# Optimization experiments

Hardware: AMD Instinct MI355X
Metric: run time of the kernel (lower is better)

## Reference

```python
import jax, jax.numpy as jnp
import numpy as np

N_NODES = 100000
N_EDGES = 3200000
D = 256
REPEAT = 2
FACTOR = 0.5


def setup_inputs() -> dict:
    key = jax.random.key(0)
    k1, k2, k3, k4, k5, k6 = jax.random.split(key, 6)
    x = jax.random.normal(k1, (N_NODES, D), dtype=jnp.float32)
    vals = jax.random.uniform(k2, (N_EDGES,), dtype=jnp.float32)
    # Xavier-ish scale for linear weights
    W0 = jax.random.normal(k3, (D, D), dtype=jnp.float32) / np.sqrt(D)
    W1 = jax.random.normal(k4, (D, D), dtype=jnp.float32) / np.sqrt(D)
    rows = jax.random.randint(k5, (N_EDGES,), 0, N_NODES, dtype=jnp.int32)
    cols = jax.random.randint(k6, (N_EDGES,), 0, N_NODES, dtype=jnp.int32)
    return {"x": x, "vals": vals, "W0": W0, "W1": W1, "rows": rows, "cols": cols}


def reference(x, vals, W0, W1, rows, cols):
    # support is sparse [N, N] in COO: support[rows[e], cols[e]] = vals[e]
    def spmm(h):
        # gather source-node features, scale by edge weight, scatter-add to dst
        return jax.ops.segment_sum(vals[:, None] * h[cols], rows,
                                   num_segments=N_NODES)

    h = x
    for W, act in ((W0, jax.nn.relu), (W1, lambda v: v)):
        # _propagate: repeated SpMM with scalar factor
        for _ in range(REPEAT):
            h = spmm(h) * FACTOR
        # linear (no bias) + activation
        h = act(h @ W)
    return h
```

## Files before the change

kernel.cpp:

```cpp
#include <hip/hip_runtime.h>
#include <hip/hip_bf16.h>
#include <hip/hip_fp16.h>

#define N_D 256
#define NBLK 832

typedef __attribute__((ext_vector_type(8))) short bf16x8;
typedef __attribute__((ext_vector_type(4))) float f32x4;
typedef __attribute__((ext_vector_type(2))) float f32x2;
typedef __attribute__((ext_vector_type(2))) int   i32x2;

__device__ __forceinline__ unsigned short f2bf(float f) {
  union { float f; unsigned u; } c; c.f = f;
  unsigned u = c.u;
  return (unsigned short)((u + 0x7fffu + ((u >> 16) & 1u)) >> 16);
}
__device__ __forceinline__ float asf(unsigned u) {
  union { unsigned u; float f; } c; c.u = u;
  return c.f;
}
__device__ __forceinline__ int grp_of(int r, unsigned gmagic) {
  int g = (int)(((unsigned long long)(unsigned)r * gmagic) >> 37);
  return min(g, 7);
}

__global__ __launch_bounds__(256) void count_kernel(
    const int* __restrict__ rows, int* __restrict__ cnt8, int* __restrict__ cntT,
    int n_edges, unsigned gmagic, int M) {
  __shared__ int lcnt[8];
  if (threadIdx.x < 8) lcnt[threadIdx.x] = 0;
  __syncthreads();
  int* __restrict__ cnt = cnt8 + (size_t)(blockIdx.x & 7) * M;
  for (int e = blockIdx.x * 256 + threadIdx.x; e < n_edges; e += NBLK * 256) {
    const int r = __builtin_nontemporal_load(&rows[e]);
    atomicAdd(&cnt[r], 1);
    atomicAdd(&lcnt[grp_of(r, gmagic)], 1);
  }
  __syncthreads();
  if (threadIdx.x < 8) cntT[threadIdx.x * NBLK + blockIdx.x] = lcnt[threadIdx.x];
}

__global__ __launch_bounds__(256) void sumcnt_kernel(
    const int* __restrict__ cnt8, int* __restrict__ cnts,
    int* __restrict__ bsum, int M) {
  __shared__ int wred[4];
  const int i = blockIdx.x * 256 + threadIdx.x;
  int s = 0;
  if (i < M) {
#pragma unroll
    for (int k = 0; k < 8; ++k) s += cnt8[(size_t)k * M + i];
    cnts[i] = s;
  }
  int t = s;
#pragma unroll
  for (int off = 32; off; off >>= 1) t += __shfl_down(t, off, 64);
  if ((threadIdx.x & 63) == 0) wred[threadIdx.x >> 6] = t;
  __syncthreads();
  if (threadIdx.x == 0) bsum[blockIdx.x] = wred[0] + wred[1] + wred[2] + wred[3];
}

__global__ __launch_bounds__(1024) void scan_kernel(
    const int* __restrict__ cnt, int* __restrict__ outA,
    int* __restrict__ outB, int n) {
  __shared__ int wsum[16];
  __shared__ int carry_sh;
  const int tid = threadIdx.x;
  const int lane = tid & 63;
  const int wid = tid >> 6;
  if (tid == 0) carry_sh = 0;
  __syncthreads();
  for (int base = 0; base < n; base += 4096) {
    const int i0 = base + tid * 4;
    int4 v = make_int4(0, 0, 0, 0);
    if (i0 + 3 < n) v = *reinterpret_cast<const int4*>(cnt + i0);
    else {
      if (i0     < n) v.x = cnt[i0];
      if (i0 + 1 < n) v.y = cnt[i0 + 1];
      if (i0 + 2 < n) v.z = cnt[i0 + 2];
    }
    const int s1 = v.x, s2 = s1 + v.y, s3 = s2 + v.z, s4 = s3 + v.w;
    int ws = s4;
#pragma unroll
    for (int off = 1; off < 64; off <<= 1) {
      int o = __shfl_up(ws, off, 64);
      if (lane >= off) ws += o;
    }
    if (lane == 63) wsum[wid] = ws;
    __syncthreads();
    if (wid == 0) {
      int t = (lane < 16) ? wsum[lane] : 0;
#pragma unroll
      for (int off = 1; off < 16; off <<= 1) {
        int o = __shfl_up(t, off, 64);
        if (lane >= off) t += o;
      }
      if (lane < 16) wsum[lane] = t;
    }
    __syncthreads();
    const int carry = carry_sh;
    const int tbase = carry + (wid ? wsum[wid - 1] : 0) + ws - s4;
    if (i0     < n) { outA[i0]     = tbase;      outB[i0]     = tbase; }
    if (i0 + 1 < n) { outA[i0 + 1] = tbase + s1; outB[i0 + 1] = tbase + s1; }
    if (i0 + 2 < n) { outA[i0 + 2] = tbase + s2; outB[i0 + 2] = tbase + s2; }
    if (i0 + 3 < n) { outA[i0 + 3] = tbase + s3; outB[i0 + 3] = tbase + s3; }
    __syncthreads();
    if (tid == 0) carry_sh = carry + wsum[15];
    __syncthreads();
  }
  if (tid == 0) outA[n] = carry_sh;
}

__global__ __launch_bounds__(256) void scan_apply_kernel(
    const int* __restrict__ cnts, const int* __restrict__ bofs,
    int* __restrict__ row_ptr, int* __restrict__ cursor, int M) {
  __shared__ int wsum[4];
  const int tid = threadIdx.x;
  const int lane = tid & 63;
  const int wid = tid >> 6;
  const int i = blockIdx.x * 256 + tid;
  const int v = (i < M) ? cnts[i] : 0;
  int s = v;
#pragma unroll
  for (int off = 1; off < 64; off <<= 1) {
    int o = __shfl_up(s, off, 64);
    if (lane >= off) s += o;
  }
  if (lane == 63) wsum[wid] = s;
  __syncthreads();
  int add = 0;
  for (int k = 0; k < wid; ++k) add += wsum[k];
  const int excl = bofs[blockIdx.x] + add + s - v;
  if (i < M) { row_ptr[i] = excl; cursor[i] = excl; }
  if (i == M) row_ptr[M] = bofs[gridDim.x];
}

__global__ __launch_bounds__(256) void partition_kernel(
    const int* __restrict__ rows, const int* __restrict__ cols,
    const float* __restrict__ vals, const int* __restrict__ pofsT,
    i32x2* __restrict__ part, int n_edges, unsigned gmagic) {
  __shared__ int lofs[8];
  if (threadIdx.x < 8) lofs[threadIdx.x] = pofsT[threadIdx.x * NBLK + blockIdx.x];
  __syncthreads();
  for (int e = blockIdx.x * 256 + threadIdx.x; e < n_edges; e += NBLK * 256) {
    const int r = __builtin_nontemporal_load(&rows[e]);
    const int c = __builtin_nontemporal_load(&cols[e]);
    const float vl = __builtin_nontemporal_load(&vals[e]);
    const int g = grp_of(r, gmagic);
    const int slot = atomicAdd(&lofs[g], 1);
    const unsigned short hb = __half_as_ushort(__float2half_rn(vl * 0.5f));
    i32x2 rv;
    rv.x = r;
    rv.y = (int)(((unsigned)c << 15) | ((unsigned)hb >> 1));
    __builtin_nontemporal_store(rv, &part[slot]);
  }
}

__global__ __launch_bounds__(256) void scatter2_kernel(
    const i32x2* __restrict__ part, const int* __restrict__ pofsT,
    int* __restrict__ cursor, unsigned* __restrict__ colpack) {
  const int g  = blockIdx.x & 7;
  const int bk = blockIdx.x >> 3;
  const int nb = gridDim.x >> 3;
  const int s0 = pofsT[g * NBLK];
  const int s1 = pofsT[(g + 1) * NBLK];
  for (int i = s0 + bk * 256 + threadIdx.x; i < s1; i += nb * 256) {
    const i32x2 rv = __builtin_nontemporal_load(&part[i]);
    const int pos = atomicAdd(&cursor[rv.x], 1);
    colpack[pos] = (unsigned)rv.y;
  }
}

template <bool RELU, bool F32OUT>
__global__ __launch_bounds__(256) void spmm_slice(
    const unsigned short* __restrict__ hin, const int* __restrict__ row_ptr,
    const unsigned* __restrict__ colpack, void* __restrict__ hout,
    int n_nodes) {
  const int slice = blockIdx.x & 3;
  const int lane = threadIdx.x & 63;
  const int half = lane >> 5;
  const int sub  = lane & 31;
  const int wgid = ((blockIdx.x >> 2) * 256 + threadIdx.x) >> 6;
  const int node = wgid * 2 + half;
  const bool ok = node < n_nodes;
  int start = 0, end = 0;
  if (ok) { start = row_ptr[node]; end = row_ptr[node + 1]; }

  const unsigned* __restrict__ hinw = reinterpret_cast<const unsigned*>(hin);
  const int fofs = slice * 32 + sub;
  const int sbase = half << 5;

  float acc0 = 0.f, acc1 = 0.f;

  for (int base = start; base < end; base += 32) {
    const int cnt = min(32, end - base);
    unsigned u = 0;
    if (base + sub < end) u = __builtin_nontemporal_load(&colpack[base + sub]);
    for (int t = 0; t < cnt; t += 16) {
      unsigned hv[16];
      float v[16];
#pragma unroll
      for (int j = 0; j < 16; ++j) {
        const unsigned ue = (unsigned)__shfl((int)u, sbase + t + j, 64);
        const int c = (int)(ue >> 15);
        v[j] = __half2float(__ushort_as_half((unsigned short)((ue & 0x7fffu) << 1)));
        hv[j] = hinw[(size_t)c * 128 + fofs];
      }
#pragma unroll
      for (int j = 0; j < 16; ++j) {
        acc0 += v[j] * asf(hv[j] << 16);
        acc1 += v[j] * asf(hv[j] & 0xffff0000u);
      }
    }
  }
  if (ok) {
    if (RELU) { acc0 = fmaxf(acc0, 0.f); acc1 = fmaxf(acc1, 0.f); }
    if (F32OUT) {
      f32x2 o; o.x = acc0; o.y = acc1;
      __builtin_nontemporal_store(o, reinterpret_cast<f32x2*>(hout) + (size_t)node * 128 + fofs);
    } else {
      unsigned o = (unsigned)f2bf(acc0) | ((unsigned)f2bf(acc1) << 16);
      __builtin_nontemporal_store(o, reinterpret_cast<unsigned*>(hout) + (size_t)node * 128 + fofs);
    }
  }
}

__global__ __launch_bounds__(256) void wconv_kernel(
    const float* __restrict__ W0, const float* __restrict__ W1,
    unsigned short* __restrict__ WT0, unsigned short* __restrict__ WT1) {
  const int w = blockIdx.x >> 8;
  const int k = blockIdx.x & 255;
  const int n = threadIdx.x;
  const float* W = w ? W1 : W0;
  unsigned short* WT = w ? WT1 : WT0;
  WT[(size_t)n * N_D + k] = f2bf(W[(size_t)k * N_D + n]);
}

template <bool AF32>
__global__ __launch_bounds__(256) void gemm2(
    const void* __restrict__ H, const unsigned short* __restrict__ WT,
    unsigned short* __restrict__ C, int M) {
  const int wave = threadIdx.x >> 6;
  const int lane = threadIdx.x & 63;
  const int m = lane & 15;
  const int p = lane >> 4;
  const int row0 = blockIdx.x * 64 + wave * 16;

  f32x4 acc[16];
#pragma unroll
  for (int i = 0; i < 16; ++i) acc[i] = (f32x4){0.f, 0.f, 0.f, 0.f};

  const int r = row0 + m;
  const bool rok = r < M;

  for (int k0 = 0; k0 < N_D; k0 += 32) {
    bf16x8 a = {0, 0, 0, 0, 0, 0, 0, 0};
    if (rok) {
      if (AF32) {
        const float* ap = (const float*)H + (size_t)r * N_D + k0 + p * 8;
        const float4 f0 = *reinterpret_cast<const float4*>(ap);
        const float4 f1 = *reinterpret_cast<const float4*>(ap + 4);
        a[0] = f2bf(f0.x); a[1] = f2bf(f0.y); a[2] = f2bf(f0.z); a[3] = f2bf(f0.w);
        a[4] = f2bf(f1.x); a[5] = f2bf(f1.y); a[6] = f2bf(f1.z); a[7] = f2bf(f1.w);
      } else {
        a = *reinterpret_cast<const bf16x8*>(
            (const unsigned short*)H + (size_t)r * N_D + k0 + p * 8);
      }
    }
#pragma unroll
    for (int nt = 0; nt < 16; ++nt) {
      const bf16x8 b = *reinterpret_cast<const bf16x8*>(
          WT + (size_t)(nt * 16 + m) * N_D + k0 + p * 8);
      acc[nt] = __builtin_amdgcn_mfma_f32_16x16x32_bf16(a, b, acc[nt], 0, 0, 0);
    }
  }

#pragma unroll
  for (int nt = 0; nt < 16; ++nt) {
    const int col = nt * 16 + m;
#pragma unroll
    for (int rr = 0; rr < 4; ++rr) {
      const int r2 = row0 + p * 4 + rr;
      if (r2 < M) {
        C[(size_t)r2 * N_D + col] = f2bf(acc[nt][rr]);
      }
    }
  }
}

extern "C" void kernel_launch(void* const* d_in, const int* in_sizes, int n_in,
                              void* d_out, int out_size, void* d_ws, size_t ws_size,
                              hipStream_t stream) {
  const float* x    = (const float*)d_in[0];
  const float* vals = (const float*)d_in[1];
  const float* W0   = (const float*)d_in[2];
  const float* W1   = (const float*)d_in[3];
  const int*   rows = (const int*)d_in[4];
  const int*   cols = (const int*)d_in[5];

  const int n_edges = in_sizes[1];
  const int M = in_sizes[0] / N_D;
  const size_t n_feat = (size_t)M * N_D;

  char* ws = (char*)d_ws;
  unsigned short* hA      = (unsigned short*)(ws);
  unsigned*       colpack = (unsigned*)(ws + 51200000);
  int*            row_ptr = (int*)(ws + 64000000);
  int*            cursor  = (int*)(ws + 64400128);
  int*            cnt8    = (int*)(ws + 64800256);
  int*            cnts    = (int*)(ws + 68000384);
  int*            bsum    = (int*)(ws + 68400512);
  int*            bofs    = (int*)(ws + 68402560);
  int*            bscr    = (int*)(ws + 68404608);
  int*            cntT    = (int*)(ws + 68406656);
  int*            pofsT   = (int*)(ws + 68433536);
  int*            pscr    = (int*)(ws + 68460416);
  unsigned short* wt0     = (unsigned short*)(ws + 68487296);
  unsigned short* wt1     = (unsigned short*)(ws + 68618368);
  unsigned short* hB   = (unsigned short*)d_out;
  unsigned short* hC   = (unsigned short*)d_out + n_feat;
  i32x2*          part = (i32x2*)((char*)d_out + 51200000);

  const int Mb = (M + 255) / 256;
  const int sblocks = 4 * ((M + 7) / 8);
  const int gblocks = (M + 63) / 64;
  const int rpg = (M + 7) / 8;
  const unsigned gmagic = (unsigned)(((1ULL << 37) + rpg - 1) / (unsigned long long)rpg);

  hipMemsetAsync(cnt8, 0, (size_t)8 * M * sizeof(int), stream);
  count_kernel<<<NBLK, 256, 0, stream>>>(rows, cnt8, cntT, n_edges, gmagic, M);
  sumcnt_kernel<<<Mb, 256, 0, stream>>>(cnt8, cnts, bsum, M);
  scan_kernel<<<1, 1024, 0, stream>>>(bsum, bofs, bscr, Mb);
  scan_apply_kernel<<<Mb, 256, 0, stream>>>(cnts, bofs, row_ptr, cursor, M);
  scan_kernel<<<1, 1024, 0, stream>>>(cntT, pofsT, pscr, 8 * NBLK);
  partition_kernel<<<NBLK, 256, 0, stream>>>(rows, cols, vals, pofsT, part,
                                             n_edges, gmagic);
  scatter2_kernel<<<NBLK, 256, 0, stream>>>(part, pofsT, cursor, colpack);
  wconv_kernel<<<512, 256, 0, stream>>>(W0, W1, wt0, wt1);

  gemm2<true ><<<gblocks, 256, 0, stream>>>(x,  wt0, hB, M);
  spmm_slice<false, false><<<sblocks, 256, 0, stream>>>(hB, row_ptr, colpack, hA, M);
  spmm_slice<true,  false><<<sblocks, 256, 0, stream>>>(hA, row_ptr, colpack, hB, M);

  gemm2<false><<<gblocks, 256, 0, stream>>>(hB, wt1, hC, M);
  spmm_slice<false, false><<<sblocks, 256, 0, stream>>>(hC, row_ptr, colpack, hA, M);
  spmm_slice<false, true ><<<sblocks, 256, 0, stream>>>(hA, row_ptr, colpack, d_out, M);
}
```

Measured before the change: 1.290 ms.

## Merge setup kernels, widen GEMM row tile, drop nontemporal hints, shrink SpMM batch

Several preprocessing launches are merged: the weight transpose runs inside the count kernel, the two scans share one two-block kernel, and the scan-apply runs alongside partitioning in one kernel. The aim is fewer launches and less serialization. The GEMM now computes 32 rows per wave so each B-fragment load feeds two MFMAs. Nontemporal loads and stores are replaced by plain accesses, and the SpMM inner gather batch shrinks from 16 to 8, which lowers register use but leaves fewer loads in flight. The half-value decode also drops its mask, relying on the 16-bit truncation.

```diff
diff --git a/kernel.cpp b/kernel.cpp
--- a/kernel.cpp
+++ b/kernel.cpp
@@ -7,8 +7,6 @@
 
 typedef __attribute__((ext_vector_type(8))) short bf16x8;
 typedef __attribute__((ext_vector_type(4))) float f32x4;
-typedef __attribute__((ext_vector_type(2))) float f32x2;
-typedef __attribute__((ext_vector_type(2))) int   i32x2;
 
 __device__ __forceinline__ unsigned short f2bf(float f) {
   union { float f; unsigned u; } c; c.f = f;
@@ -24,15 +22,27 @@
   return min(g, 7);
 }
 
-__global__ __launch_bounds__(256) void count_kernel(
+__global__ __launch_bounds__(256) void build1_kernel(
     const int* __restrict__ rows, int* __restrict__ cnt8, int* __restrict__ cntT,
-    int n_edges, unsigned gmagic, int M) {
+    int n_edges, unsigned gmagic, int M,
+    const float* __restrict__ W0, const float* __restrict__ W1,
+    unsigned short* __restrict__ WT0, unsigned short* __restrict__ WT1) {
+  if (blockIdx.x >= NBLK) {
+    const int b = blockIdx.x - NBLK;
+    const int w = b >> 8;
+    const int k = b & 255;
+    const int n = threadIdx.x;
+    const float* W = w ? W1 : W0;
+    unsigned short* WT = w ? WT1 : WT0;
+    WT[(size_t)n * N_D + k] = f2bf(W[(size_t)k * N_D + n]);
+    return;
+  }
   __shared__ int lcnt[8];
   if (threadIdx.x < 8) lcnt[threadIdx.x] = 0;
   __syncthreads();
   int* __restrict__ cnt = cnt8 + (size_t)(blockIdx.x & 7) * M;
   for (int e = blockIdx.x * 256 + threadIdx.x; e < n_edges; e += NBLK * 256) {
-    const int r = __builtin_nontemporal_load(&rows[e]);
+    const int r = rows[e];
     atomicAdd(&cnt[r], 1);
     atomicAdd(&lcnt[grp_of(r, gmagic)], 1);
   }
@@ -59,24 +69,22 @@
   if (threadIdx.x == 0) bsum[blockIdx.x] = wred[0] + wred[1] + wred[2] + wred[3];
 }
 
-__global__ __launch_bounds__(1024) void scan_kernel(
-    const int* __restrict__ cnt, int* __restrict__ outA,
-    int* __restrict__ outB, int n) {
-  __shared__ int wsum[16];
+__device__ void scan256(const int* __restrict__ in, int* __restrict__ out, int n) {
+  __shared__ int wsum[4];
   __shared__ int carry_sh;
   const int tid = threadIdx.x;
   const int lane = tid & 63;
   const int wid = tid >> 6;
   if (tid == 0) carry_sh = 0;
   __syncthreads();
-  for (int base = 0; base < n; base += 4096) {
+  for (int base = 0; base < n; base += 1024) {
     const int i0 = base + tid * 4;
     int4 v = make_int4(0, 0, 0, 0);
-    if (i0 + 3 < n) v = *reinterpret_cast<const int4*>(cnt + i0);
+    if (i0 + 3 < n) v = *reinterpret_cast<const int4*>(in + i0);
     else {
-      if (i0     < n) v.x = cnt[i0];
-      if (i0 + 1 < n) v.y = cnt[i0 + 1];
-      if (i0 + 2 < n) v.z = cnt[i0 + 2];
+      if (i0     < n) v.x = in[i0];
+      if (i0 + 1 < n) v.y = in[i0 + 1];
+      if (i0 + 2 < n) v.z = in[i0 + 2];
     }
     const int s1 = v.x, s2 = s1 + v.y, s3 = s2 + v.z, s4 = s3 + v.w;
     int ws = s4;
@@ -88,75 +96,80 @@
     if (lane == 63) wsum[wid] = ws;
     __syncthreads();
     if (wid == 0) {
-      int t = (lane < 16) ? wsum[lane] : 0;
-#pragma unroll
-      for (int off = 1; off < 16; off <<= 1) {
+      int t = (lane < 4) ? wsum[lane] : 0;
+#pragma unroll
+      for (int off = 1; off < 4; off <<= 1) {
         int o = __shfl_up(t, off, 64);
         if (lane >= off) t += o;
       }
-      if (lane < 16) wsum[lane] = t;
+      if (lane < 4) wsum[lane] = t;
     }
     __syncthreads();
     const int carry = carry_sh;
     const int tbase = carry + (wid ? wsum[wid - 1] : 0) + ws - s4;
-    if (i0     < n) { outA[i0]     = tbase;      outB[i0]     = tbase; }
-    if (i0 + 1 < n) { outA[i0 + 1] = tbase + s1; outB[i0 + 1] = tbase + s1; }
-    if (i0 + 2 < n) { outA[i0 + 2] = tbase + s2; outB[i0 + 2] = tbase + s2; }
-    if (i0 + 3 < n) { outA[i0 + 3] = tbase + s3; outB[i0 + 3] = tbase + s3; }
-    __syncthreads();
-    if (tid == 0) carry_sh = carry + wsum[15];
-    __syncthreads();
-  }
-  if (tid == 0) outA[n] = carry_sh;
-}
-
-__global__ __launch_bounds__(256) void scan_apply_kernel(
+    if (i0     < n) out[i0]     = tbase;
+    if (i0 + 1 < n) out[i0 + 1] = tbase + s1;
+    if (i0 + 2 < n) out[i0 + 2] = tbase + s2;
+    if (i0 + 3 < n) out[i0 + 3] = tbase + s3;
+    __syncthreads();
+    if (tid == 0) carry_sh = carry + wsum[3];
+    __syncthreads();
+  }
+  if (tid == 0) out[n] = carry_sh;
+}
+
+__global__ __launch_bounds__(256) void scan2_kernel(
+    const int* __restrict__ bsum, int* __restrict__ bofs, int Mb,
+    const int* __restrict__ cntT, int* __restrict__ pofsT) {
+  if (blockIdx.x == 0) scan256(bsum, bofs, Mb);
+  else                 scan256(cntT, pofsT, 8 * NBLK);
+}
+
+__global__ __launch_bounds__(256) void build2_kernel(
     const int* __restrict__ cnts, const int* __restrict__ bofs,
-    int* __restrict__ row_ptr, int* __restrict__ cursor, int M) {
-  __shared__ int wsum[4];
-  const int tid = threadIdx.x;
-  const int lane = tid & 63;
-  const int wid = tid >> 6;
-  const int i = blockIdx.x * 256 + tid;
-  const int v = (i < M) ? cnts[i] : 0;
-  int s = v;
-#pragma unroll
-  for (int off = 1; off < 64; off <<= 1) {
-    int o = __shfl_up(s, off, 64);
-    if (lane >= off) s += o;
-  }
-  if (lane == 63) wsum[wid] = s;
-  __syncthreads();
-  int add = 0;
-  for (int k = 0; k < wid; ++k) add += wsum[k];
-  const int excl = bofs[blockIdx.x] + add + s - v;
-  if (i < M) { row_ptr[i] = excl; cursor[i] = excl; }
-  if (i == M) row_ptr[M] = bofs[gridDim.x];
-}
-
-__global__ __launch_bounds__(256) void partition_kernel(
+    int* __restrict__ row_ptr, int* __restrict__ cursor, int M, int Mb,
     const int* __restrict__ rows, const int* __restrict__ cols,
     const float* __restrict__ vals, const int* __restrict__ pofsT,
-    i32x2* __restrict__ part, int n_edges, unsigned gmagic) {
-  __shared__ int lofs[8];
-  if (threadIdx.x < 8) lofs[threadIdx.x] = pofsT[threadIdx.x * NBLK + blockIdx.x];
-  __syncthreads();
-  for (int e = blockIdx.x * 256 + threadIdx.x; e < n_edges; e += NBLK * 256) {
-    const int r = __builtin_nontemporal_load(&rows[e]);
-    const int c = __builtin_nontemporal_load(&cols[e]);
-    const float vl = __builtin_nontemporal_load(&vals[e]);
-    const int g = grp_of(r, gmagic);
-    const int slot = atomicAdd(&lofs[g], 1);
-    const unsigned short hb = __half_as_ushort(__float2half_rn(vl * 0.5f));
-    i32x2 rv;
-    rv.x = r;
-    rv.y = (int)(((unsigned)c << 15) | ((unsigned)hb >> 1));
-    __builtin_nontemporal_store(rv, &part[slot]);
+    int2* __restrict__ part, int n_edges, unsigned gmagic) {
+  __shared__ int shmem[8];
+  if (blockIdx.x < Mb) {
+    const int tid = threadIdx.x;
+    const int lane = tid & 63;
+    const int wid = tid >> 6;
+    const int i = blockIdx.x * 256 + tid;
+    const int v = (i < M) ? cnts[i] : 0;
+    int s = v;
+#pragma unroll
+    for (int off = 1; off < 64; off <<= 1) {
+      int o = __shfl_up(s, off, 64);
+      if (lane >= off) s += o;
+    }
+    if (lane == 63) shmem[wid] = s;
+    __syncthreads();
+    int add = 0;
+    for (int k = 0; k < wid; ++k) add += shmem[k];
+    const int excl = bofs[blockIdx.x] + add + s - v;
+    if (i < M) { row_ptr[i] = excl; cursor[i] = excl; }
+    if (i == M) row_ptr[M] = bofs[Mb];
+  } else {
+    const int pb = blockIdx.x - Mb;
+    if (threadIdx.x < 8) shmem[threadIdx.x] = pofsT[threadIdx.x * NBLK + pb];
+    __syncthreads();
+    for (int e = pb * 256 + threadIdx.x; e < n_edges; e += NBLK * 256) {
+      const int r = rows[e];
+      const int g = grp_of(r, gmagic);
+      const int slot = atomicAdd(&shmem[g], 1);
+      const unsigned short hb = __half_as_ushort(__float2half_rn(vals[e] * 0.5f));
+      int2 rv;
+      rv.x = r;
+      rv.y = (int)(((unsigned)cols[e] << 15) | ((unsigned)hb >> 1));
+      part[slot] = rv;
+    }
   }
 }
 
 __global__ __launch_bounds__(256) void scatter2_kernel(
-    const i32x2* __restrict__ part, const int* __restrict__ pofsT,
+    const int2* __restrict__ part, const int* __restrict__ pofsT,
     int* __restrict__ cursor, unsigned* __restrict__ colpack) {
   const int g  = blockIdx.x & 7;
   const int bk = blockIdx.x >> 3;
@@ -164,7 +177,7 @@
   const int s0 = pofsT[g * NBLK];
   const int s1 = pofsT[(g + 1) * NBLK];
   for (int i = s0 + bk * 256 + threadIdx.x; i < s1; i += nb * 256) {
-    const i32x2 rv = __builtin_nontemporal_load(&part[i]);
+    const int2 rv = part[i];
     const int pos = atomicAdd(&cursor[rv.x], 1);
     colpack[pos] = (unsigned)rv.y;
   }
@@ -195,18 +208,18 @@
     const int cnt = min(32, end - base);
     unsigned u = 0;
     if (base + sub < end) u = __builtin_nontemporal_load(&colpack[base + sub]);
-    for (int t = 0; t < cnt; t += 16) {
-      unsigned hv[16];
-      float v[16];
-#pragma unroll
-      for (int j = 0; j < 16; ++j) {
+    for (int t = 0; t < cnt; t += 8) {
+      unsigned hv[8];
+      float v[8];
+#pragma unroll
+      for (int j = 0; j < 8; ++j) {
         const unsigned ue = (unsigned)__shfl((int)u, sbase + t + j, 64);
         const int c = (int)(ue >> 15);
-        v[j] = __half2float(__ushort_as_half((unsigned short)((ue & 0x7fffu) << 1)));
+        v[j] = __half2float(__ushort_as_half((unsigned short)(ue << 1)));
         hv[j] = hinw[(size_t)c * 128 + fofs];
       }
 #pragma unroll
-      for (int j = 0; j < 16; ++j) {
+      for (int j = 0; j < 8; ++j) {
         acc0 += v[j] * asf(hv[j] << 16);
         acc1 += v[j] * asf(hv[j] & 0xffff0000u);
       }
@@ -215,62 +228,65 @@
   if (ok) {
     if (RELU) { acc0 = fmaxf(acc0, 0.f); acc1 = fmaxf(acc1, 0.f); }
     if (F32OUT) {
-      f32x2 o; o.x = acc0; o.y = acc1;
-      __builtin_nontemporal_store(o, reinterpret_cast<f32x2*>(hout) + (size_t)node * 128 + fofs);
+      reinterpret_cast<float2*>(hout)[(size_t)node * 128 + fofs] =
+          make_float2(acc0, acc1);
     } else {
-      unsigned o = (unsigned)f2bf(acc0) | ((unsigned)f2bf(acc1) << 16);
-      __builtin_nontemporal_store(o, reinterpret_cast<unsigned*>(hout) + (size_t)node * 128 + fofs);
-    }
-  }
-}
-
-__global__ __launch_bounds__(256) void wconv_kernel(
-    const float* __restrict__ W0, const float* __restrict__ W1,
-    unsigned short* __restrict__ WT0, unsigned short* __restrict__ WT1) {
-  const int w = blockIdx.x >> 8;
-  const int k = blockIdx.x & 255;
-  const int n = threadIdx.x;
-  const float* W = w ? W1 : W0;
-  unsigned short* WT = w ? WT1 : WT0;
-  WT[(size_t)n * N_D + k] = f2bf(W[(size_t)k * N_D + n]);
+      reinterpret_cast<unsigned*>(hout)[(size_t)node * 128 + fofs] =
+          (unsigned)f2bf(acc0) | ((unsigned)f2bf(acc1) << 16);
+    }
+  }
 }
 
 template <bool AF32>
-__global__ __launch_bounds__(256) void gemm2(
+__global__ __launch_bounds__(256) void gemm3(
     const void* __restrict__ H, const unsigned short* __restrict__ WT,
     unsigned short* __restrict__ C, int M) {
   const int wave = threadIdx.x >> 6;
   const int lane = threadIdx.x & 63;
   const int m = lane & 15;
   const int p = lane >> 4;
-  const int row0 = blockIdx.x * 64 + wave * 16;
-
-  f32x4 acc[16];
-#pragma unroll
-  for (int i = 0; i < 16; ++i) acc[i] = (f32x4){0.f, 0.f, 0.f, 0.f};
-
-  const int r = row0 + m;
-  const bool rok = r < M;
+  const int row0 = blockIdx.x * 128 + wave * 32;
+
+  f32x4 acc0[16], acc1[16];
+#pragma unroll
+  for (int i = 0; i < 16; ++i) {
+    acc0[i] = (f32x4){0.f, 0.f, 0.f, 0.f};
+    acc1[i] = (f32x4){0.f, 0.f, 0.f, 0.f};
+  }
+
+  const int r0 = row0 + m;
+  const int r1 = row0 + 16 + m;
+  const bool ok0 = r0 < M, ok1 = r1 < M;
 
   for (int k0 = 0; k0 < N_D; k0 += 32) {
-    bf16x8 a = {0, 0, 0, 0, 0, 0, 0, 0};
-    if (rok) {
-      if (AF32) {
-        const float* ap = (const float*)H + (size_t)r * N_D + k0 + p * 8;
+    bf16x8 a0 = {0,0,0,0,0,0,0,0}, a1 = {0,0,0,0,0,0,0,0};
+    if (AF32) {
+      if (ok0) {
+        const float* ap = (const float*)H + (size_t)r0 * N_D + k0 + p * 8;
         const float4 f0 = *reinterpret_cast<const float4*>(ap);
         const float4 f1 = *reinterpret_cast<const float4*>(ap + 4);
-        a[0] = f2bf(f0.x); a[1] = f2bf(f0.y); a[2] = f2bf(f0.z); a[3] = f2bf(f0.w);
-        a[4] = f2bf(f1.x); a[5] = f2bf(f1.y); a[6] = f2bf(f1.z); a[7] = f2bf(f1.w);
-      } else {
-        a = *reinterpret_cast<const bf16x8*>(
-            (const unsigned short*)H + (size_t)r * N_D + k0 + p * 8);
-      }
+        a0[0]=f2bf(f0.x); a0[1]=f2bf(f0.y); a0[2]=f2bf(f0.z); a0[3]=f2bf(f0.w);
+        a0[4]=f2bf(f1.x); a0[5]=f2bf(f1.y); a0[6]=f2bf(f1.z); a0[7]=f2bf(f1.w);
+      }
+      if (ok1) {
+        const float* ap = (const float*)H + (size_t)r1 * N_D + k0 + p * 8;
+        const float4 f0 = *reinterpret_cast<const float4*>(ap);
+        const float4 f1 = *reinterpret_cast<const float4*>(ap + 4);
+        a1[0]=f2bf(f0.x); a1[1]=f2bf(f0.y); a1[2]=f2bf(f0.z); a1[3]=f2bf(f0.w);
+        a1[4]=f2bf(f1.x); a1[5]=f2bf(f1.y); a1[6]=f2bf(f1.z); a1[7]=f2bf(f1.w);
+      }
+    } else {
+      if (ok0) a0 = *reinterpret_cast<const bf16x8*>(
+          (const unsigned short*)H + (size_t)r0 * N_D + k0 + p * 8);
+      if (ok1) a1 = *reinterpret_cast<const bf16x8*>(
+          (const unsigned short*)H + (size_t)r1 * N_D + k0 + p * 8);
     }
 #pragma unroll
     for (int nt = 0; nt < 16; ++nt) {
       const bf16x8 b = *reinterpret_cast<const bf16x8*>(
           WT + (size_t)(nt * 16 + m) * N_D + k0 + p * 8);
-      acc[nt] = __builtin_amdgcn_mfma_f32_16x16x32_bf16(a, b, acc[nt], 0, 0, 0);
+      acc0[nt] = __builtin_amdgcn_mfma_f32_16x16x32_bf16(a0, b, acc0[nt], 0, 0, 0);
+      acc1[nt] = __builtin_amdgcn_mfma_f32_16x16x32_bf16(a1, b, acc1[nt], 0, 0, 0);
     }
   }
 
@@ -279,10 +295,10 @@
     const int col = nt * 16 + m;
 #pragma unroll
     for (int rr = 0; rr < 4; ++rr) {
-      const int r2 = row0 + p * 4 + rr;
-      if (r2 < M) {
-        C[(size_t)r2 * N_D + col] = f2bf(acc[nt][rr]);
-      }
+      const int ra = row0 + p * 4 + rr;
+      const int rb = ra + 16;
+      if (ra < M) C[(size_t)ra * N_D + col] = f2bf(acc0[nt][rr]);
+      if (rb < M) C[(size_t)rb * N_D + col] = f2bf(acc1[nt][rr]);
     }
   }
 }
@@ -310,38 +326,35 @@
   int*            cnts    = (int*)(ws + 68000384);
   int*            bsum    = (int*)(ws + 68400512);
   int*            bofs    = (int*)(ws + 68402560);
-  int*            bscr    = (int*)(ws + 68404608);
   int*            cntT    = (int*)(ws + 68406656);
   int*            pofsT   = (int*)(ws + 68433536);
-  int*            pscr    = (int*)(ws + 68460416);
   unsigned short* wt0     = (unsigned short*)(ws + 68487296);
   unsigned short* wt1     = (unsigned short*)(ws + 68618368);
   unsigned short* hB   = (unsigned short*)d_out;
   unsigned short* hC   = (unsigned short*)d_out + n_feat;
-  i32x2*          part = (i32x2*)((char*)d_out + 51200000);
+  int2*           part = (int2*)((char*)d_out + 51200000);
 
   const int Mb = (M + 255) / 256;
   const int sblocks = 4 * ((M + 7) / 8);
-  const int gblocks = (M + 63) / 64;
+  const int gblocks = (M + 127) / 128;
   const int rpg = (M + 7) / 8;
   const unsigned gmagic = (unsigned)(((1ULL << 37) + rpg - 1) / (unsigned long long)rpg);
 
   hipMemsetAsync(cnt8, 0, (size_t)8 * M * sizeof(int), stream);
-  count_kernel<<<NBLK, 256, 0, stream>>>(rows, cnt8, cntT, n_edges, gmagic, M);
+  build1_kernel<<<NBLK + 512, 256, 0, stream>>>(rows, cnt8, cntT, n_edges, gmagic, M,
+                                                W0, W1, wt0, wt1);
   sumcnt_kernel<<<Mb, 256, 0, stream>>>(cnt8, cnts, bsum, M);
-  scan_kernel<<<1, 1024, 0, stream>>>(bsum, bofs, bscr, Mb);
-  scan_apply_kernel<<<Mb, 256, 0, stream>>>(cnts, bofs, row_ptr, cursor, M);
-  scan_kernel<<<1, 1024, 0, stream>>>(cntT, pofsT, pscr, 8 * NBLK);
-  partition_kernel<<<NBLK, 256, 0, stream>>>(rows, cols, vals, pofsT, part,
-                                             n_edges, gmagic);
+  scan2_kernel<<<2, 256, 0, stream>>>(bsum, bofs, Mb, cntT, pofsT);
+  build2_kernel<<<Mb + NBLK, 256, 0, stream>>>(cnts, bofs, row_ptr, cursor, M, Mb,
+                                               rows, cols, vals, pofsT, part,
+                                               n_edges, gmagic);
   scatter2_kernel<<<NBLK, 256, 0, stream>>>(part, pofsT, cursor, colpack);
-  wconv_kernel<<<512, 256, 0, stream>>>(W0, W1, wt0, wt1);
-
-  gemm2<true ><<<gblocks, 256, 0, stream>>>(x,  wt0, hB, M);
+
+  gemm3<true ><<<gblocks, 256, 0, stream>>>(x,  wt0, hB, M);
   spmm_slice<false, false><<<sblocks, 256, 0, stream>>>(hB, row_ptr, colpack, hA, M);
   spmm_slice<true,  false><<<sblocks, 256, 0, stream>>>(hA, row_ptr, colpack, hB, M);
 
-  gemm2<false><<<gblocks, 256, 0, stream>>>(hB, wt1, hC, M);
+  gemm3<false><<<gblocks, 256, 0, stream>>>(hB, wt1, hC, M);
   spmm_slice<false, false><<<sblocks, 256, 0, stream>>>(hC, row_ptr, colpack, hA, M);
   spmm_slice<false, true ><<<sblocks, 256, 0, stream>>>(hA, row_ptr, colpack, d_out, M);
 }
```

Result: faster. 1.235 ms (-4.3%).
